# Performance work log

Measured on AMD Instinct MI355X. Metric: run time of the kernel, lower is better.

The kernel has to match this reference:

```python
import jax, jax.numpy as jnp
import numpy as np

SLEN, BSZ, D_MODEL, N_HEAD, D_HEAD, PROJ_DIM = 2048, 2, 1024, 16, 64, 256
LN_EPS = 1e-5
PRIME_EPS = 1e-4


def setup_inputs() -> dict:
    key = jax.random.key(0)
    ks = jax.random.split(key, 4)
    h = jax.random.normal(ks[0], (SLEN, BSZ, D_MODEL), jnp.float32)
    W_qkvb = jax.random.normal(ks[1], (D_MODEL, N_HEAD * (3 * D_HEAD + 1)), jnp.float32) * (D_MODEL ** -0.5)
    W_o = jax.random.normal(ks[2], (N_HEAD * D_HEAD, D_MODEL), jnp.float32) * ((N_HEAD * D_HEAD) ** -0.5)
    ln_gamma = jnp.ones((D_MODEL,), jnp.float32)
    ln_beta = jnp.zeros((D_MODEL,), jnp.float32)
    # orthogonal random matrix (d_head, proj_dim): blocks of orthonormal cols, rows scaled to norm sqrt(d)
    rng = np.random.default_rng(0)
    blocks = []
    for _ in range(PROJ_DIM // D_HEAD):
        qm, _ = np.linalg.qr(rng.standard_normal((D_HEAD, D_HEAD)))
        blocks.append(qm)
    pm = np.concatenate(blocks, axis=1) * np.sqrt(D_HEAD)
    proj_matrix = jnp.asarray(pm, jnp.float32)  # (d_head, proj_dim)
    return {"h": h, "W_qkvb": W_qkvb, "W_o": W_o, "ln_gamma": ln_gamma,
            "ln_beta": ln_beta, "proj_matrix": proj_matrix}


def prime(x, pm):
    # FAVOR+ hyperbolic softmax-kernel features. x: (B,H,L,d), pm: (d,m) -> (B,H,L,2m)
    d = x.shape[-1]
    m = pm.shape[-1]
    xn = x * (d ** -0.25)
    proj = jnp.einsum('bhld,dm->bhlm', xn, pm)
    hnorm = 0.5 * jnp.sum(xn * xn, axis=-1, keepdims=True)
    feat = jnp.concatenate([jnp.exp(proj - hnorm), jnp.exp(-proj - hnorm)], axis=-1)
    return ((2 * m) ** -0.5) * (feat + PRIME_EPS)


def layer_norm(x, gamma, beta):
    mu = jnp.mean(x, axis=-1, keepdims=True)
    var = jnp.mean(jnp.square(x - mu), axis=-1, keepdims=True)
    return (x - mu) * jax.lax.rsqrt(var + LN_EPS) * gamma + beta


def reference(h, W_qkvb, W_o, ln_gamma, ln_beta, proj_matrix):
    slen, bsz, _ = h.shape
    qkvb = (h @ W_qkvb).reshape(slen, bsz, N_HEAD, 3 * D_HEAD + 1)
    q, k, v, hb = jnp.split(qkvb, [D_HEAD, 2 * D_HEAD, 3 * D_HEAD], axis=-1)
    hb = jax.nn.sigmoid(hb)
    # (L,B,H,*) -> (B,H,L,*)
    q = q.transpose(1, 2, 0, 3)
    k = k.transpose(1, 2, 0, 3)
    v = v.transpose(1, 2, 0, 3)
    hb = hb.transpose(1, 2, 0, 3)
    qp = prime(q, proj_matrix)
    kp = prime(k, proj_matrix)
    kp = kp / kp.sum(-1, keepdims=True)
    qp = qp / qp.sum(-1, keepdims=True)
    # time-major for the scan: (L,B,H,*)
    qpT = qp.transpose(2, 0, 1, 3)
    kpT = kp.transpose(2, 0, 1, 3)
    vT = v.transpose(2, 0, 1, 3)
    hbT = hb.transpose(2, 0, 1, 3)
    W0 = jnp.zeros((bsz, N_HEAD, 2 * PROJ_DIM, D_HEAD), h.dtype)

    def step(W, inp):
        qt, kt, vt, bt = inp  # (B,H,2m),(B,H,2m),(B,H,d),(B,H,1)
        v_old = jnp.einsum('bhpd,bhp->bhd', W, kt)
        W = W + jnp.einsum('bhp,bhd->bhpd', kt, bt * (vt - v_old))
        out = jnp.einsum('bhpd,bhp->bhd', W, qt)
        return W, out

    _, outs = jax.lax.scan(step, W0, (qpT, kpT, vT, hbT))  # outs: (L,B,H,d)
    scale = D_HEAD ** -0.5
    layer_out = (scale * outs).reshape(slen, bsz, N_HEAD * D_HEAD)
    attn_out = layer_out @ W_o
    return layer_norm(h + attn_out, ln_gamma, ln_beta)
```

## Files before the change

### kernel.cpp

```cpp
#include <hip/hip_runtime.h>
#include <hip/hip_bf16.h>

#define LSEQ   2048
#define BSZN   2
#define DMODEL 1024
#define NHEAD  16
#define DH     64
#define MPROJ  256
#define PF     512
#define CHK    64
#define NCHK   32
#define BHN    32
#define NQKV   3088
#define NQPAD  3200

typedef __hip_bfloat16 bf16;
typedef short bf16x8 __attribute__((ext_vector_type(8)));
typedef float f32x4 __attribute__((ext_vector_type(4)));

#define MFMA(a, b, c) __builtin_amdgcn_mfma_f32_16x16x32_bf16(a, b, c, 0, 0, 0)

#define UNP(u, a, b) { a = __uint_as_float((unsigned)(u) << 16); b = __uint_as_float((unsigned)(u) & 0xffff0000u); }

static __device__ __forceinline__ float b2f(bf16 x) {
  unsigned short us = *(unsigned short*)&x;
  return __uint_as_float((unsigned)us << 16);
}
static __device__ __forceinline__ bf16 f2b(float x) { return __float2bfloat16(x); }
static __device__ __forceinline__ unsigned pkbf(float a, float b) {
  bf16 x = __float2bfloat16(a), y = __float2bfloat16(b);
  return ((unsigned)(*(unsigned short*)&y) << 16) | (unsigned)(*(unsigned short*)&x);
}

static __device__ __forceinline__ void gl_lds16(const void* gsrc, void* ldst) {
  __builtin_amdgcn_global_load_lds(
      (const __attribute__((address_space(1))) unsigned int*)gsrc,
      (__attribute__((address_space(3))) unsigned int*)ldst, 16, 0, 0);
}

#define MEMFENCE asm volatile("" ::: "memory")
#define WAITV(n) asm volatile("s_waitcnt vmcnt(" #n ")" ::: "memory")
#define WAITLGKM asm volatile("s_waitcnt lgkmcnt(0)" ::: "memory")
#define BARRIER() __builtin_amdgcn_s_barrier()

__global__ __launch_bounds__(256)
void k_cvth(const float* __restrict__ h, bf16* __restrict__ hbf)
{
  const int gt = blockIdx.x * 256 + threadIdx.x;
  const int r = gt >> 7, ug = gt & 127;
  const int grp = ug >> 3, u = ug & 7;
  const float4 f0 = *(const float4*)&h[(size_t)r * 1024 + grp * 64 + u * 8];
  const float4 f1 = *(const float4*)&h[(size_t)r * 1024 + grp * 64 + u * 8 + 4];
  uint4 o;
  o.x = pkbf(f0.x, f0.y); o.y = pkbf(f0.z, f0.w);
  o.z = pkbf(f1.x, f1.y); o.w = pkbf(f1.z, f1.w);
  *(uint4*)&hbf[(size_t)r * 1024 + grp * 64 + ((u ^ (r & 7)) << 3)] = o;
}

__global__ __launch_bounds__(256)
void k_cvtw(const float* __restrict__ W, bf16* __restrict__ WT, int nsrc)
{
  __shared__ float sT[64][65];
  const int tid = threadIdx.x;
  const int n0 = blockIdx.x * 64, k0 = blockIdx.y * 64;
#pragma unroll
  for (int j = 0; j < 16; j++) {
    const int e = j * 256 + tid;
    const int r = e >> 6, c = e & 63;
    sT[r][c] = (n0 + c < nsrc) ? W[(size_t)(k0 + r) * nsrc + n0 + c] : 0.f;
  }
  __syncthreads();
#pragma unroll
  for (int j = 0; j < 2; j++) {
    const int uid = j * 256 + tid;
    const int rp = uid >> 3, u = uid & 7;
    uint4 o;
    o.x = pkbf(sT[u * 8 + 0][rp], sT[u * 8 + 1][rp]);
    o.y = pkbf(sT[u * 8 + 2][rp], sT[u * 8 + 3][rp]);
    o.z = pkbf(sT[u * 8 + 4][rp], sT[u * 8 + 5][rp]);
    o.w = pkbf(sT[u * 8 + 6][rp], sT[u * 8 + 7][rp]);
    *(uint4*)&WT[(size_t)(n0 + rp) * 1024 + k0 + ((u ^ (rp & 7)) << 3)] = o;
  }
}

__global__ __launch_bounds__(256)
void k_cvtpm(const float* __restrict__ pm, bf16* __restrict__ pmThi,
             bf16* __restrict__ pmTlo)
{
  const int n = threadIdx.x;
  float v[64];
#pragma unroll
  for (int d = 0; d < 64; d++) v[d] = pm[d * MPROJ + n] * 0.35355339059327373f;
  const int key = n & 7;
#pragma unroll
  for (int u = 0; u < 8; u++) {
    unsigned hi[4], lo[4];
#pragma unroll
    for (int j = 0; j < 4; j++) {
      const float a = v[u * 8 + j * 2], b = v[u * 8 + j * 2 + 1];
      const bf16 ah = f2b(a), bh_ = f2b(b);
      const float ar = a - b2f(ah), br = b - b2f(bh_);
      hi[j] = ((unsigned)(*(const unsigned short*)&bh_) << 16) | (unsigned)(*(const unsigned short*)&ah);
      const bf16 al = f2b(ar), bl = f2b(br);
      lo[j] = ((unsigned)(*(const unsigned short*)&bl) << 16) | (unsigned)(*(const unsigned short*)&al);
    }
    *(uint4*)&pmThi[(size_t)n * 64 + ((u ^ key) << 3)] = make_uint4(hi[0], hi[1], hi[2], hi[3]);
    *(uint4*)&pmTlo[(size_t)n * 64 + ((u ^ key) << 3)] = make_uint4(lo[0], lo[1], lo[2], lo[3]);
  }
}

#define GEMM_STAGE(Abase, Bbase, kt, b) {                                      \
  const size_t kb = (size_t)(kt) * 128;           \
  _Pragma("unroll")                                                            \
  for (int j = 0; j < 4; j++) {                                                \
    const int row = (w * 4 + j) * 8 + (lane >> 3);                             \
    gl_lds16((const char*)(Abase) + (size_t)(m0 + row) * 2048 + kb + (lane & 7) * 16, \
             &sA[b][(w * 4 + j) * 1024]);                                      \
  }                                                                            \
  _Pragma("unroll")                                                            \
  for (int j = 0; j < 4; j++) {                                                \
    const int row = (w * 4 + j) * 8 + (lane >> 3);                             \
    gl_lds16((const char*)(Bbase) + (size_t)(n0 + row) * 2048 + kb + (lane & 7) * 16, \
             &sB[b][(w * 4 + j) * 1024]);                                      \
  } }

#define GEMM_COMPUTE(b) {                                                      \
  _Pragma("unroll")                                                            \
  for (int ks = 0; ks < 2; ks++) {                                             \
    bf16x8 af[4], bfr[4];                                                      \
    _Pragma("unroll")                                                          \
    for (int f = 0; f < 4; f++) {                                              \
      const int row = wm * 64 + f * 16 + l16;                                  \
      af[f] = *(const bf16x8*)&sA[b][row * 128 + (((ks * 4 + lg) ^ xs) << 4)]; \
    }                                                                          \
    _Pragma("unroll")                                                          \
    for (int f = 0; f < 4; f++) {                                              \
      const int row = wn * 64 + f * 16 + l16;                                  \
      bfr[f] = *(const bf16x8*)&sB[b][row * 128 + (((ks * 4 + lg) ^ xs) << 4)]; \
    }                                                                          \
    _Pragma("unroll")                                                          \
    for (int fm = 0; fm < 4; fm++)                                             \
      _Pragma("unroll")                                                        \
      for (int fn = 0; fn < 4; fn++)                                           \
        acc[fm][fn] = MFMA(af[fm], bfr[fn], acc[fm][fn]);                      \
  } }

#define GEMM_PREAMBLE                                                          \
  __shared__ __align__(16) char sA[2][16384];                                  \
  __shared__ __align__(16) char sB[2][16384];                                  \
  const int tid = threadIdx.x, w = tid >> 6, lane = tid & 63;                  \
  const int l16 = lane & 15, lg = lane >> 4;                                   \
  const int wm = w >> 1, wn = w & 1;                                           \
  const int m0 = blockIdx.y * 128, n0 = blockIdx.x * 128;                      \
  const int xs = l16 & 7;                                                      \
  f32x4 acc[4][4];                                                             \
  _Pragma("unroll")                                                            \
  for (int i = 0; i < 4; i++)                                                  \
    _Pragma("unroll")                                                          \
    for (int j = 0; j < 4; j++) acc[i][j] = (f32x4){0.f, 0.f, 0.f, 0.f};

__global__ __launch_bounds__(256, 2)
void k_gemm_qkvb(const bf16* __restrict__ A, const bf16* __restrict__ B,
                 bf16* __restrict__ qh, bf16* __restrict__ kh,
                 bf16* __restrict__ vh, float* __restrict__ bbuf)
{
  GEMM_PREAMBLE
  GEMM_STAGE(A, B, 0, 0);
  __syncthreads();
  for (int kt = 0; kt < 16; kt++) {
    const int b = kt & 1;
    if (kt < 15) GEMM_STAGE(A, B, kt + 1, b ^ 1);
    GEMM_COMPUTE(b);
    __syncthreads();
  }
#pragma unroll
  for (int fm = 0; fm < 4; fm++)
#pragma unroll
    for (int fn = 0; fn < 4; fn++)
#pragma unroll
      for (int reg = 0; reg < 4; reg++) {
        const int m = m0 + wm * 64 + fm * 16 + lg * 4 + reg;
        const int n = n0 + wn * 64 + fn * 16 + l16;
        if (n >= NQKV) continue;
        const float v = acc[fm][fn][reg];
        const int l = m >> 1, bidx = m & 1;
        const int hd = n / 193;
        const int rem = n - hd * 193;
        const int bhi = bidx * NHEAD + hd;
        const size_t o = ((size_t)bhi * LSEQ + l) * DH;
        if (rem < 64) {
          const int d = rem;
          qh[o + ((((d >> 3) ^ (l & 7)) << 3) | (d & 7))] = f2b(v);
        } else if (rem < 128) {
          const int d = rem - 64;
          kh[o + ((((d >> 3) ^ (l & 7)) << 3) | (d & 7))] = f2b(v);
        } else if (rem < 192) {
          vh[o + rem - 128] = f2b(v);
        } else {
          bbuf[(size_t)bhi * LSEQ + l] = 1.f / (1.f + __expf(-v));
        }
      }
}

__global__ __launch_bounds__(256, 2)
void k_gemm_out(const bf16* __restrict__ A, const bf16* __restrict__ B,
                const float* __restrict__ h, float* __restrict__ ao)
{
  GEMM_PREAMBLE
  GEMM_STAGE(A, B, 0, 0);
  __syncthreads();
  for (int kt = 0; kt < 16; kt++) {
    const int b = kt & 1;
    if (kt < 15) GEMM_STAGE(A, B, kt + 1, b ^ 1);
    GEMM_COMPUTE(b);
    __syncthreads();
  }
#pragma unroll
  for (int fm = 0; fm < 4; fm++)
#pragma unroll
    for (int fn = 0; fn < 4; fn++)
#pragma unroll
      for (int reg = 0; reg < 4; reg++) {
        const int m = m0 + wm * 64 + fm * 16 + lg * 4 + reg;
        const int n = n0 + wn * 64 + fn * 16 + l16;
        const size_t o = (size_t)m * DMODEL + n;
        ao[o] = acc[fm][fn][reg] + h[o];
      }
}

__global__ __launch_bounds__(256, 2)
void k_featm(const bf16* __restrict__ qh, const bf16* __restrict__ kh,
             const bf16* __restrict__ pmThi, const bf16* __restrict__ pmTlo,
             bf16* __restrict__ Qp, bf16* __restrict__ Kp)
{
  __shared__ __align__(16) char sPM[2][32768];
  __shared__ __align__(16) char sX[8192];

  const int tid = threadIdx.x, w = tid >> 6, lane = tid & 63;
  const int l16 = lane & 15, lg = lane >> 4;
  const int xs = l16 & 7;
  const int l0 = blockIdx.x * 64, bhi = blockIdx.y;

#pragma unroll
  for (int j = 0; j < 8; j++)
    gl_lds16((const char*)pmThi + (size_t)(w * 8 + j) * 1024 + lane * 16,
             &sPM[0][(w * 8 + j) * 1024]);
#pragma unroll
  for (int j = 0; j < 8; j++)
    gl_lds16((const char*)pmTlo + (size_t)(w * 8 + j) * 1024 + lane * 16,
             &sPM[1][(w * 8 + j) * 1024]);
  {
    const char* qb = (const char*)(qh + ((size_t)bhi * LSEQ + l0) * DH);
#pragma unroll
    for (int j = 0; j < 2; j++)
      gl_lds16(qb + (size_t)(w * 2 + j) * 1024 + lane * 16, &sX[(w * 2 + j) * 1024]);
  }
  MEMFENCE;
  WAITV(0); BARRIER();

  const int srow = w * 16 + l16;
  const size_t gsr = (size_t)bhi * LSEQ + l0 + srow;

  for (int wh = 0; wh < 2; wh++) {
    bf16* dst = wh ? Kp : Qp;

    float hn;
    {
      const char* xrow = &sX[srow * 128];
      const uint4 a0 = *(const uint4*)&xrow[lg * 32];
      const uint4 a1 = *(const uint4*)&xrow[lg * 32 + 16];
      float f0, f1, f2, f3, f4, f5, f6, f7, a = 0.f;
      UNP(a0.x, f0, f1); UNP(a0.y, f2, f3); UNP(a0.z, f4, f5); UNP(a0.w, f6, f7);
      a = fmaf(f0, f0, a); a = fmaf(f1, f1, a); a = fmaf(f2, f2, a); a = fmaf(f3, f3, a);
      a = fmaf(f4, f4, a); a = fmaf(f5, f5, a); a = fmaf(f6, f6, a); a = fmaf(f7, f7, a);
      UNP(a1.x, f0, f1); UNP(a1.y, f2, f3); UNP(a1.z, f4, f5); UNP(a1.w, f6, f7);
      a = fmaf(f0, f0, a); a = fmaf(f1, f1, a); a = fmaf(f2, f2, a); a = fmaf(f3, f3, a);
      a = fmaf(f4, f4, a); a = fmaf(f5, f5, a); a = fmaf(f6, f6, a); a = fmaf(f7, f7, a);
      a += __shfl_xor(a, 16); a += __shfl_xor(a, 32);
      hn = a * 0.0625f;
    }

    f32x4 acc[16];
#pragma unroll
    for (int i = 0; i < 16; i++) acc[i] = (f32x4){0.f, 0.f, 0.f, 0.f};
#pragma unroll
    for (int ks = 0; ks < 2; ks++) {
      const bf16x8 bx = *(const bf16x8*)&sX[srow * 128 + (((ks * 4 + lg) ^ xs) << 4)];
#pragma unroll
      for (int mt = 0; mt < 16; mt++) {
        const bf16x8 ah = *(const bf16x8*)&sPM[0][(mt * 16 + l16) * 128 + (((ks * 4 + lg) ^ xs) << 4)];
        acc[mt] = MFMA(ah, bx, acc[mt]);
        const bf16x8 al = *(const bf16x8*)&sPM[1][(mt * 16 + l16) * 128 + (((ks * 4 + lg) ^ xs) << 4)];
        acc[mt] = MFMA(al, bx, acc[mt]);
      }
    }

    if (wh == 0) {
      BARRIER();
      const char* kb = (const char*)(kh + ((size_t)bhi * LSEQ + l0) * DH);
#pragma unroll
      for (int j = 0; j < 2; j++)
        gl_lds16(kb + (size_t)(w * 2 + j) * 1024 + lane * 16, &sX[(w * 2 + j) * 1024]);
      MEMFENCE;
    }

    float ss = 0.f;
#pragma unroll
    for (int mt = 0; mt < 16; mt++)
#pragma unroll
      for (int r = 0; r < 4; r++) {
        const float p = acc[mt][r];
        ss += __expf(p - hn) + __expf(-p - hn);
      }
    ss += __shfl_xor(ss, 16); ss += __shfl_xor(ss, 32);
    const float D = ss + 0.0512f;
    const float cc = 1e-4f / D;
    const float eo = hn + __logf(D);

    const size_t gb = gsr * PF;
    const int half = (lg & 1) * 4;
    const int ub = lg >> 1;
#pragma unroll
    for (int mt = 0; mt < 16; mt++) {
      const float v0 = __expf(acc[mt][0] - eo) + cc;
      const float v1 = __expf(acc[mt][1] - eo) + cc;
      const float v2 = __expf(acc[mt][2] - eo) + cc;
      const float v3 = __expf(acc[mt][3] - eo) + cc;
      const float n0 = __expf(-acc[mt][0] - eo) + cc;
      const float n1 = __expf(-acc[mt][1] - eo) + cc;
      const float n2 = __expf(-acc[mt][2] - eo) + cc;
      const float n3 = __expf(-acc[mt][3] - eo) + cc;
      const int u = mt * 2 + ub;
      *(uint2*)&dst[gb + ((u ^ xs) << 3) + half] = make_uint2(pkbf(v0, v1), pkbf(v2, v3));
      *(uint2*)&dst[gb + (((u + 32) ^ xs) << 3) + half] = make_uint2(pkbf(n0, n1), pkbf(n2, n3));
      __builtin_amdgcn_sched_barrier(0);
    }

    if (wh == 0) { WAITV(32); BARRIER(); }
  }
}

__global__ __launch_bounds__(256, 2)
void k_sgsolve(const bf16* __restrict__ Kp, const bf16* __restrict__ Qp,
               const float* __restrict__ bbuf,
               bf16* __restrict__ Gl, bf16* __restrict__ Tm,
               bf16* __restrict__ KpT)
{
  __shared__ __align__(16) char bufK[2][8192];
  __shared__ __align__(16) char bufQ[2][8192];
  __shared__ float sS[CHK][65];
  __shared__ float sT[CHK][65];
  __shared__ float sBeta[CHK];

  const int tid = threadIdx.x, w = tid >> 6, lane = tid & 63;
  const int l16 = lane & 15, lg = lane >> 4;
  const int xs = l16 & 7;
  const int c = blockIdx.x, bhi = blockIdx.y;
  const size_t cb = ((size_t)bhi * LSEQ + (size_t)c * CHK) * PF;
  const size_t rowb = (size_t)bhi * LSEQ + (size_t)c * CHK;
  const size_t ktb = (((size_t)bhi * NCHK + c) * 512) * 64;
  const size_t sb = (((size_t)bhi * NCHK + c) * CHK) * CHK;

  if (tid < CHK) sBeta[tid] = bbuf[rowb + tid];

  f32x4 accS[4], accG[4];
#pragma unroll
  for (int i = 0; i < 4; i++) { accS[i] = (f32x4){0.f,0.f,0.f,0.f}; accG[i] = (f32x4){0.f,0.f,0.f,0.f}; }

#define SG_STAGE(win, b) {                                                     \
  _Pragma("unroll")                                                            \
  for (int j = 0; j < 2; j++) {                                                \
    const int row = w * 16 + j * 8 + (lane >> 3);                              \
    gl_lds16((const char*)(Kp + cb) + (size_t)row * 1024 + (size_t)(win) * 128 + (lane & 7) * 16, \
             &bufK[b][(w * 16 + j * 8) * 128]);                                \
  }                                                                            \
  _Pragma("unroll")                                                            \
  for (int j = 0; j < 2; j++) {                                                \
    const int row = w * 16 + j * 8 + (lane >> 3);                              \
    gl_lds16((const char*)(Qp + cb) + (size_t)row * 1024 + (size_t)(win) * 128 + (lane & 7) * 16, \
             &bufQ[b][(w * 16 + j * 8) * 128]);                                \
  } }

  SG_STAGE(0, 0);
  MEMFENCE;

  for (int win = 0; win < 8; win++) {
    const int b = win & 1;
    if (win < 7) { SG_STAGE(win + 1, b ^ 1); MEMFENCE; }
    if (win == 0)      { WAITV(4); }
    else if (win < 7)  { WAITV(6); }
    else               { WAITV(2); }
    BARRIER();

#pragma unroll
    for (int ks = 0; ks < 2; ks++) {
      const bf16x8 aK = *(const bf16x8*)&bufK[b][(16 * w + l16) * 128 + (((ks * 4 + lg) ^ xs) << 4)];
      const bf16x8 aQ = *(const bf16x8*)&bufQ[b][(16 * w + l16) * 128 + (((ks * 4 + lg) ^ xs) << 4)];
      bf16x8 bK[4];
#pragma unroll
      for (int nt = 0; nt < 4; nt++)
        bK[nt] = *(const bf16x8*)&bufK[b][(nt * 16 + l16) * 128 + (((ks * 4 + lg) ^ xs) << 4)];
#pragma unroll
      for (int nt = 0; nt < 4; nt++) {
        accS[nt] = MFMA(aK, bK[nt], accS[nt]);
        accG[nt] = MFMA(aQ, bK[nt], accG[nt]);
      }
    }

#pragma unroll
    for (int jj = 0; jj < 2; jj++) {
      const int idx = jj * 256 + tid;
      const int pl = idx >> 3, l8 = idx & 7;
      unsigned short v[8];
#pragma unroll
      for (int j = 0; j < 8; j++) {
        const int l = l8 * 8 + j;
        v[j] = *(const unsigned short*)&bufK[b][l * 128 + (((pl >> 3) ^ (l & 7)) << 4) + (pl & 7) * 2];
      }
      uint4 o;
      o.x = ((unsigned)v[1] << 16) | v[0];
      o.y = ((unsigned)v[3] << 16) | v[2];
      o.z = ((unsigned)v[5] << 16) | v[4];
      o.w = ((unsigned)v[7] << 16) | v[6];
      const int p = win * 64 + pl;
      *(uint4*)&KpT[ktb + (size_t)p * 64 + ((l8 ^ (p & 7)) << 3)] = o;
    }
    BARRIER();
  }
#undef SG_STAGE

#pragma unroll
  for (int nt = 0; nt < 4; nt++)
#pragma unroll
    for (int reg = 0; reg < 4; reg++) {
      const int ri = 16 * w + lg * 4 + reg;
      const int cj = nt * 16 + l16;
      sS[ri][cj] = accS[nt][reg];
      Gl[sb + ri * 64 + (((cj >> 3) ^ (ri & 7)) << 3) + (cj & 7)] =
          f2b((cj <= ri) ? accG[nt][reg] : 0.f);
    }
  __syncthreads();

  if (tid < CHK) {
    const int j = tid;
    for (int i = 0; i < CHK; i++) {
      float acc = (i == j) ? 1.f : 0.f;
      for (int k = 0; k < i; k++) acc = fmaf(-sS[i][k], sT[k][j], acc);
      sT[i][j] = sBeta[i] * acc;
    }
  }
  __syncthreads();
  for (int t = tid; t < CHK * CHK; t += 256) {
    const int r = t >> 6, ccj = t & 63;
    Tm[sb + r * 64 + (((ccj >> 3) ^ (r & 7)) << 3) + (ccj & 7)] = f2b(sT[r][ccj]);
  }
}

__global__ __launch_bounds__(512, 2)
void k_scan(const bf16* __restrict__ Kp, const bf16* __restrict__ Qp,
            const bf16* __restrict__ vh, const bf16* __restrict__ Tm,
            const bf16* __restrict__ Gl, const bf16* __restrict__ KpT,
            bf16* __restrict__ lobf)
{
  __shared__ __align__(16) char sWT[16384];
  __shared__ __align__(16) char suP[2048];
  __shared__ __align__(16) char sUT[2048];
  __shared__ __align__(16) float pbuf[4][16][16];

  const int tid = threadIdx.x;
  const int w = tid >> 6, lane = tid & 63;
  const int l16 = lane & 15, lg = lane >> 4;
  const int wp = w >> 1, h = w & 1;
  const int bhi = blockIdx.x & 31, dq = blockIdx.x >> 5;
  const int bidx = bhi >> 4, hd = bhi & 15;
  const int xs = l16 & 7;
  const int trow = 16 * wp + l16;

  for (int i = tid; i < 4096; i += 512) ((unsigned*)sWT)[i] = 0u;

  f32x4 Wacc[4];
#pragma unroll
  for (int i = 0; i < 4; i++) Wacc[i] = (f32x4){0.f, 0.f, 0.f, 0.f};

  const size_t bh_base = (size_t)bhi * LSEQ * PF;
  const size_t tg0 = ((size_t)bhi * NCHK) * 4096;
  const size_t kt0 = ((size_t)bhi * NCHK) * (512 * 64);

  const bf16* KpF = Kp + bh_base + (size_t)trow * PF + h * 256;
  const bf16* QpF = Qp + bh_base + (size_t)trow * PF + h * 256;
  const bf16* KTF = KpT + kt0 + (size_t)(64 * w + l16) * 64;

  bf16x8 fKp[8], fQp[8], fKT[8];
  bf16x8 tf0 = {}, tf1 = {}, gf0 = {}, gf1 = {};
  float v0 = 0.f, v1 = 0.f, v2 = 0.f, v3 = 0.f;

#define LOADKP(c) { const bf16* _b = KpF + (size_t)(c) * CHK * PF;             \
  _Pragma("unroll")                                                            \
  for (int ks = 0; ks < 8; ks++)                                               \
    fKp[ks] = *(const bf16x8*)(_b + (((ks * 4 + lg) ^ xs) << 3)); }
#define LOADQP(c) { const bf16* _b = QpF + (size_t)(c) * CHK * PF;             \
  _Pragma("unroll")                                                            \
  for (int ks = 0; ks < 8; ks++)                                               \
    fQp[ks] = *(const bf16x8*)(_b + (((ks * 4 + lg) ^ xs) << 3)); }
#define LOADKT(c) { const bf16* _b = KTF + (size_t)(c) * (512 * 64);           \
  _Pragma("unroll")                                                            \
  for (int mt = 0; mt < 4; mt++) {                                             \
    fKT[mt * 2]     = *(const bf16x8*)(_b + mt * 16 * 64 + (((    lg) ^ xs) << 3)); \
    fKT[mt * 2 + 1] = *(const bf16x8*)(_b + mt * 16 * 64 + (((4 + lg) ^ xs) << 3)); \
  } }
#define LOADTG(c) if (!h) {                                                    \
  const bf16* _t = Tm + tg0 + (size_t)(c) * 4096;                              \
  const bf16* _g = Gl + tg0 + (size_t)(c) * 4096;                              \
  tf0 = *(const bf16x8*)&_t[trow * 64 + ((lg ^ xs) << 3)];                     \
  tf1 = *(const bf16x8*)&_t[trow * 64 + (((4 + lg) ^ xs) << 3)];               \
  gf0 = *(const bf16x8*)&_g[trow * 64 + ((lg ^ xs) << 3)];                     \
  gf1 = *(const bf16x8*)&_g[trow * 64 + (((4 + lg) ^ xs) << 3)];               \
  const bf16* _v = vh + ((size_t)bhi * LSEQ + (c) * 64 + wp * 16 + lg * 4) * 64 + dq * 16 + l16; \
  v0 = b2f(_v[0]); v1 = b2f(_v[64]); v2 = b2f(_v[128]); v3 = b2f(_v[192]); }

  LOADKP(0); LOADKT(0); LOADQP(0); LOADTG(0);
  WAITLGKM; BARRIER();

  for (int c = 0; c < NCHK; c++) {
    BARRIER();

    f32x4 a0v = (f32x4){0.f,0.f,0.f,0.f}, a1v = (f32x4){0.f,0.f,0.f,0.f};
    bf16x8 wb[8];
#pragma unroll
    for (int ks = 0; ks < 8; ks += 2) {
      wb[ks] = *(const bf16x8*)&sWT[l16 * 1024 + (((h * 32 + ks * 4 + lg) ^ xs) << 4)];
      a0v = MFMA(fKp[ks], wb[ks], a0v);
      wb[ks + 1] = *(const bf16x8*)&sWT[l16 * 1024 + (((h * 32 + (ks + 1) * 4 + lg) ^ xs) << 4)];
      a1v = MFMA(fKp[ks + 1], wb[ks + 1], a1v);
    }
    if (c < NCHK - 1) LOADKP(c + 1);
    if (h) {
      float4 pv;
      pv.x = a0v[0] + a1v[0]; pv.y = a0v[1] + a1v[1];
      pv.z = a0v[2] + a1v[2]; pv.w = a0v[3] + a1v[3];
      *(float4*)&pbuf[wp][l16][lg * 4] = pv;
    }
    WAITLGKM; BARRIER();

    if (!h) {
      const float4 po = *(const float4*)&pbuf[wp][l16][lg * 4];
      const float u0 = v0 - (a0v[0] + a1v[0]) - po.x;
      const float u1 = v1 - (a0v[1] + a1v[1]) - po.y;
      const float u2 = v2 - (a0v[2] + a1v[2]) - po.z;
      const float u3 = v3 - (a0v[3] + a1v[3]) - po.w;
      const int l0r = 16 * wp + lg * 4;
      *(uint2*)&suP[l16 * 128 + (((l0r >> 3) ^ xs) << 4) + (l0r & 7) * 2] =
          make_uint2(pkbf(u0, u1), pkbf(u2, u3));
    }
    WAITLGKM; BARRIER();

    if (!h) {
      f32x4 ua = (f32x4){0.f,0.f,0.f,0.f};
      ua = MFMA(tf0, *(const bf16x8*)&suP[l16 * 128 + ((lg ^ xs) << 4)], ua);
      ua = MFMA(tf1, *(const bf16x8*)&suP[l16 * 128 + (((4 + lg) ^ xs) << 4)], ua);
      const int l0r = 16 * wp + lg * 4;
      *(uint2*)&sUT[l16 * 128 + (((l0r >> 3) ^ xs) << 4) + (l0r & 7) * 2] =
          make_uint2(pkbf(ua[0], ua[1]), pkbf(ua[2], ua[3]));
    }
    WAITLGKM; BARRIER();

    const bf16x8 bu0 = *(const bf16x8*)&sUT[l16 * 128 + ((lg ^ xs) << 4)];
    const bf16x8 bu1 = *(const bf16x8*)&sUT[l16 * 128 + (((4 + lg) ^ xs) << 4)];
#pragma unroll
    for (int mt = 0; mt < 4; mt++) {
      Wacc[mt] = MFMA(fKT[mt * 2], bu0, Wacc[mt]);
      Wacc[mt] = MFMA(fKT[mt * 2 + 1], bu1, Wacc[mt]);
    }
    if (c < NCHK - 1) LOADKT(c + 1);
#pragma unroll
    for (int mt = 0; mt < 4; mt++) {
      const int p0m = w * 64 + mt * 16 + lg * 4;
      *(uint2*)&sWT[l16 * 1024 + (((p0m >> 3) ^ xs) << 4) + (p0m & 7) * 2] =
          make_uint2(pkbf(Wacc[mt][0], Wacc[mt][1]), pkbf(Wacc[mt][2], Wacc[mt][3]));
    }

    f32x4 o0 = (f32x4){0.f,0.f,0.f,0.f}, o1 = (f32x4){0.f,0.f,0.f,0.f};
#pragma unroll
    for (int ks = 0; ks < 8; ks += 2) {
      o0 = MFMA(fQp[ks], wb[ks], o0);
      o1 = MFMA(fQp[ks + 1], wb[ks + 1], o1);
    }
    if (c < NCHK - 1) LOADQP(c + 1);
    if (h) {
      float4 pv;
      pv.x = o0[0] + o1[0]; pv.y = o0[1] + o1[1];
      pv.z = o0[2] + o1[2]; pv.w = o0[3] + o1[3];
      *(float4*)&pbuf[wp][l16][lg * 4] = pv;
    } else {
      o0 = MFMA(gf0, bu0, o0);
      o1 = MFMA(gf1, bu1, o1);
    }
    WAITLGKM; BARRIER();

    if (!h) {
      const float4 po = *(const float4*)&pbuf[wp][l16][lg * 4];
      const float pr4[4] = {po.x, po.y, po.z, po.w};
      const int colb = hd * 64 + dq * 16 + l16;
#pragma unroll
      for (int reg = 0; reg < 4; reg++) {
        const int l = c * 64 + 16 * wp + lg * 4 + reg;
        const int r = l * BSZN + bidx;
        const int cp = (colb & ~63) | ((((colb >> 3) & 7) ^ (r & 7)) << 3) | (colb & 7);
        lobf[(size_t)r * DMODEL + cp] = f2b(0.125f * (o0[reg] + o1[reg] + pr4[reg]));
      }
    }
    if (c < NCHK - 1) LOADTG(c + 1);
    WAITLGKM;
  }
#undef LOADKP
#undef LOADQP
#undef LOADKT
#undef LOADTG
}

__global__ __launch_bounds__(256)
void k_ln(const float* __restrict__ ao, const float* __restrict__ gamma,
          const float* __restrict__ beta, float* __restrict__ out)
{
  const int row = blockIdx.x;
  const int tid = threadIdx.x;
  __shared__ float r1[4], r2[4];
  const float4 v = *(const float4*)&ao[(size_t)row * DMODEL + tid * 4];
  float s1 = v.x + v.y + v.z + v.w;
  float s2 = v.x * v.x + v.y * v.y + v.z * v.z + v.w * v.w;
  for (int off = 32; off > 0; off >>= 1) {
    s1 += __shfl_down(s1, off);
    s2 += __shfl_down(s2, off);
  }
  if ((tid & 63) == 0) { r1[tid >> 6] = s1; r2[tid >> 6] = s2; }
  __syncthreads();
  const float ts1 = r1[0] + r1[1] + r1[2] + r1[3];
  const float ts2 = r2[0] + r2[1] + r2[2] + r2[3];
  const float mu = ts1 * (1.f / DMODEL);
  const float var = ts2 * (1.f / DMODEL) - mu * mu;
  const float rs = rsqrtf(var + 1e-5f);
  const float4 g = *(const float4*)&gamma[tid * 4];
  const float4 b = *(const float4*)&beta[tid * 4];
  float4 o;
  o.x = (v.x - mu) * rs * g.x + b.x;
  o.y = (v.y - mu) * rs * g.y + b.y;
  o.z = (v.z - mu) * rs * g.z + b.z;
  o.w = (v.w - mu) * rs * g.w + b.w;
  *(float4*)&out[(size_t)row * DMODEL + tid * 4] = o;
}

extern "C" void kernel_launch(void* const* d_in, const int* in_sizes, int n_in,
                              void* d_out, int out_size, void* d_ws, size_t ws_size,
                              hipStream_t stream)
{
  (void)in_sizes; (void)n_in; (void)out_size; (void)ws_size;
  const float* h   = (const float*)d_in[0];
  const float* Wq  = (const float*)d_in[1];
  const float* Wo  = (const float*)d_in[2];
  const float* gam = (const float*)d_in[3];
  const float* bet = (const float*)d_in[4];
  const float* pm  = (const float*)d_in[5];
  float* out = (float*)d_out;

  char* ws = (char*)d_ws;
  size_t off = 0;
  auto alloc = [&](size_t bytes) -> void* {
    void* p = ws + off;
    off += (bytes + 255) & ~(size_t)255;
    return p;
  };
  bf16*  vh  = (bf16*)alloc((size_t)BHN * LSEQ * DH * 2);
  float* bbf = (float*)alloc((size_t)BHN * LSEQ * 4);
  bf16*  Kp  = (bf16*)alloc((size_t)BHN * LSEQ * PF * 2);
  bf16*  Qp  = (bf16*)alloc((size_t)BHN * LSEQ * PF * 2);
  bf16*  Tm  = (bf16*)alloc((size_t)BHN * NCHK * CHK * CHK * 2);
  bf16*  Gll = (bf16*)alloc((size_t)BHN * NCHK * CHK * CHK * 2);
  char*  R   = (char*)alloc((size_t)BHN * NCHK * 512 * 64 * 2);
  bf16*  WoT = (bf16*)alloc((size_t)DMODEL * DMODEL * 2);
  bf16*  pmThi = (bf16*)alloc((size_t)MPROJ * 64 * 2);
  bf16*  pmTlo = (bf16*)alloc((size_t)MPROJ * 64 * 2);
  bf16*  qh  = (bf16*)R;
  bf16*  kh  = (bf16*)(R + (size_t)BHN * LSEQ * DH * 2);
  bf16*  hbf = (bf16*)(R + (size_t)2 * BHN * LSEQ * DH * 2);
  bf16*  WqT = (bf16*)(R + (size_t)3 * BHN * LSEQ * DH * 2);
  bf16*  KpT = (bf16*)R;
  float* ao  = (float*)R;
  bf16*  lobf = (bf16*)d_out;

  k_cvth     <<<dim3(2048),                       256, 0, stream>>>(h, hbf);
  k_cvtw     <<<dim3(NQPAD / 64, 16),             256, 0, stream>>>(Wq, WqT, NQKV);
  k_cvtw     <<<dim3(DMODEL / 64, 16),            256, 0, stream>>>(Wo, WoT, DMODEL);
  k_cvtpm    <<<dim3(1),                          256, 0, stream>>>(pm, pmThi, pmTlo);
  k_gemm_qkvb<<<dim3(NQPAD / 128, 4096 / 128),    256, 0, stream>>>(hbf, WqT, qh, kh, vh, bbf);
  k_featm    <<<dim3(LSEQ / 64, BHN),             256, 0, stream>>>(qh, kh, pmThi, pmTlo, Qp, Kp);
  k_sgsolve  <<<dim3(NCHK, BHN),                  256, 0, stream>>>(Kp, Qp, bbf, Gll, Tm, KpT);
  k_scan     <<<dim3(128),                        512, 0, stream>>>(Kp, Qp, vh, Tm, Gll, KpT, lobf);
  k_gemm_out <<<dim3(DMODEL / 128, 4096 / 128),   256, 0, stream>>>(lobf, WoT, h, ao);
  k_ln       <<<dim3(4096),                       256, 0, stream>>>(ao, gam, bet, out);
}
```

Measured before the change: 379.5 us.

## Compute the T·u product redundantly per wave to drop scan barriers

In the chunked delta-rule scan, every wave now computes the full 64x64 T·u product itself from a per-wave copy of T held in registers. It writes the result to its own LDS scratch slot instead of a shared buffer filled by half the waves. This removes one block-wide barrier per chunk. The loop-top barrier is also dropped, and the partial-sum buffer is double-buffered so the two uses within an iteration do not conflict. The cost is more MFMA work and loads per chunk, extra LDS, and about 32 extra VGPRs under a (512,2) launch bound, which could cause spills or lower occupancy.

After: 501.3 us. 1.32x slower.

```diff
diff --git a/kernel.cpp b/kernel.cpp
--- a/kernel.cpp
+++ b/kernel.cpp
@@ -464,8 +464,8 @@
 {
   __shared__ __align__(16) char sWT[16384];
   __shared__ __align__(16) char suP[2048];
-  __shared__ __align__(16) char sUT[2048];
-  __shared__ __align__(16) float pbuf[4][16][16];
+  __shared__ __align__(16) char uScr[8][2048];
+  __shared__ __align__(16) float pbuf[2][4][16][16];
 
   const int tid = threadIdx.x;
   const int w = tid >> 6, lane = tid & 63;
@@ -490,8 +490,8 @@
   const bf16* QpF = Qp + bh_base + (size_t)trow * PF + h * 256;
   const bf16* KTF = KpT + kt0 + (size_t)(64 * w + l16) * 64;
 
-  bf16x8 fKp[8], fQp[8], fKT[8];
-  bf16x8 tf0 = {}, tf1 = {}, gf0 = {}, gf1 = {};
+  bf16x8 fKp[8], fQp[8], fKT[8], tf[8];
+  bf16x8 gf0 = {}, gf1 = {};
   float v0 = 0.f, v1 = 0.f, v2 = 0.f, v3 = 0.f;
 
 #define LOADKP(c) { const bf16* _b = KpF + (size_t)(c) * CHK * PF;             \
@@ -508,22 +508,23 @@
     fKT[mt * 2]     = *(const bf16x8*)(_b + mt * 16 * 64 + (((    lg) ^ xs) << 3)); \
     fKT[mt * 2 + 1] = *(const bf16x8*)(_b + mt * 16 * 64 + (((4 + lg) ^ xs) << 3)); \
   } }
-#define LOADTG(c) if (!h) {                                                    \
-  const bf16* _t = Tm + tg0 + (size_t)(c) * 4096;                              \
+#define LOADT(c) { const bf16* _t = Tm + tg0 + (size_t)(c) * 4096;             \
+  _Pragma("unroll")                                                            \
+  for (int t = 0; t < 4; t++) {                                                \
+    tf[t * 2]     = *(const bf16x8*)&_t[(t * 16 + l16) * 64 + (((    lg) ^ xs) << 3)]; \
+    tf[t * 2 + 1] = *(const bf16x8*)&_t[(t * 16 + l16) * 64 + (((4 + lg) ^ xs) << 3)]; \
+  } }
+#define LOADVG(c) if (!h) {                                                    \
   const bf16* _g = Gl + tg0 + (size_t)(c) * 4096;                              \
-  tf0 = *(const bf16x8*)&_t[trow * 64 + ((lg ^ xs) << 3)];                     \
-  tf1 = *(const bf16x8*)&_t[trow * 64 + (((4 + lg) ^ xs) << 3)];               \
   gf0 = *(const bf16x8*)&_g[trow * 64 + ((lg ^ xs) << 3)];                     \
   gf1 = *(const bf16x8*)&_g[trow * 64 + (((4 + lg) ^ xs) << 3)];               \
   const bf16* _v = vh + ((size_t)bhi * LSEQ + (c) * 64 + wp * 16 + lg * 4) * 64 + dq * 16 + l16; \
   v0 = b2f(_v[0]); v1 = b2f(_v[64]); v2 = b2f(_v[128]); v3 = b2f(_v[192]); }
 
-  LOADKP(0); LOADKT(0); LOADQP(0); LOADTG(0);
+  LOADKP(0); LOADKT(0); LOADQP(0); LOADT(0); LOADVG(0);
   WAITLGKM; BARRIER();
 
   for (int c = 0; c < NCHK; c++) {
-    BARRIER();
-
     f32x4 a0v = (f32x4){0.f,0.f,0.f,0.f}, a1v = (f32x4){0.f,0.f,0.f,0.f};
     bf16x8 wb[8];
 #pragma unroll
@@ -538,12 +539,12 @@
       float4 pv;
       pv.x = a0v[0] + a1v[0]; pv.y = a0v[1] + a1v[1];
       pv.z = a0v[2] + a1v[2]; pv.w = a0v[3] + a1v[3];
-      *(float4*)&pbuf[wp][l16][lg * 4] = pv;
+      *(float4*)&pbuf[0][wp][l16][lg * 4] = pv;
     }
     WAITLGKM; BARRIER();
 
     if (!h) {
-      const float4 po = *(const float4*)&pbuf[wp][l16][lg * 4];
+      const float4 po = *(const float4*)&pbuf[0][wp][l16][lg * 4];
       const float u0 = v0 - (a0v[0] + a1v[0]) - po.x;
       const float u1 = v1 - (a0v[1] + a1v[1]) - po.y;
       const float u2 = v2 - (a0v[2] + a1v[2]) - po.z;
@@ -554,18 +555,29 @@
     }
     WAITLGKM; BARRIER();
 
-    if (!h) {
-      f32x4 ua = (f32x4){0.f,0.f,0.f,0.f};
-      ua = MFMA(tf0, *(const bf16x8*)&suP[l16 * 128 + ((lg ^ xs) << 4)], ua);
-      ua = MFMA(tf1, *(const bf16x8*)&suP[l16 * 128 + (((4 + lg) ^ xs) << 4)], ua);
-      const int l0r = 16 * wp + lg * 4;
-      *(uint2*)&sUT[l16 * 128 + (((l0r >> 3) ^ xs) << 4) + (l0r & 7) * 2] =
-          make_uint2(pkbf(ua[0], ua[1]), pkbf(ua[2], ua[3]));
-    }
-    WAITLGKM; BARRIER();
-
-    const bf16x8 bu0 = *(const bf16x8*)&sUT[l16 * 128 + ((lg ^ xs) << 4)];
-    const bf16x8 bu1 = *(const bf16x8*)&sUT[l16 * 128 + (((4 + lg) ^ xs) << 4)];
+    {
+      const bf16x8 sp0 = *(const bf16x8*)&suP[l16 * 128 + ((lg ^ xs) << 4)];
+      const bf16x8 sp1 = *(const bf16x8*)&suP[l16 * 128 + (((4 + lg) ^ xs) << 4)];
+      f32x4 ua[4];
+#pragma unroll
+      for (int t = 0; t < 4; t++) {
+        ua[t] = (f32x4){0.f, 0.f, 0.f, 0.f};
+        ua[t] = MFMA(tf[t * 2], sp0, ua[t]);
+        ua[t] = MFMA(tf[t * 2 + 1], sp1, ua[t]);
+      }
+      if (c < NCHK - 1) LOADT(c + 1);
+      char* scr = uScr[w];
+#pragma unroll
+      for (int t = 0; t < 4; t++) {
+        const int lout = t * 16 + lg * 4;
+        *(uint2*)&scr[l16 * 128 + (((lout >> 3) ^ xs) << 4) + (lout & 7) * 2] =
+            make_uint2(pkbf(ua[t][0], ua[t][1]), pkbf(ua[t][2], ua[t][3]));
+      }
+    }
+    WAITLGKM;
+    const bf16x8 bu0 = *(const bf16x8*)&uScr[w][l16 * 128 + ((lg ^ xs) << 4)];
+    const bf16x8 bu1 = *(const bf16x8*)&uScr[w][l16 * 128 + (((4 + lg) ^ xs) << 4)];
+
 #pragma unroll
     for (int mt = 0; mt < 4; mt++) {
       Wacc[mt] = MFMA(fKT[mt * 2], bu0, Wacc[mt]);
@@ -590,7 +602,7 @@
       float4 pv;
       pv.x = o0[0] + o1[0]; pv.y = o0[1] + o1[1];
       pv.z = o0[2] + o1[2]; pv.w = o0[3] + o1[3];
-      *(float4*)&pbuf[wp][l16][lg * 4] = pv;
+      *(float4*)&pbuf[1][wp][l16][lg * 4] = pv;
     } else {
       o0 = MFMA(gf0, bu0, o0);
       o1 = MFMA(gf1, bu1, o1);
@@ -598,7 +610,7 @@
     WAITLGKM; BARRIER();
 
     if (!h) {
-      const float4 po = *(const float4*)&pbuf[wp][l16][lg * 4];
+      const float4 po = *(const float4*)&pbuf[1][wp][l16][lg * 4];
       const float pr4[4] = {po.x, po.y, po.z, po.w};
       const int colb = hd * 64 + dq * 16 + l16;
 #pragma unroll
@@ -609,13 +621,13 @@
         lobf[(size_t)r * DMODEL + cp] = f2b(0.125f * (o0[reg] + o1[reg] + pr4[reg]));
       }
     }
-    if (c < NCHK - 1) LOADTG(c + 1);
-    WAITLGKM;
+    if (c < NCHK - 1) LOADVG(c + 1);
   }
 #undef LOADKP
 #undef LOADQP
 #undef LOADKT
-#undef LOADTG
+#undef LOADT
+#undef LOADVG
 }
 
 __global__ __launch_bounds__(256)
```
